# Optimization experiments

Measured on AMD Instinct MI355X. Metric: run time of the kernel, lower is better.

## Reference

```python
import jax, jax.numpy as jnp
import numpy as np

CI_SCALE = 1.0


def _rot_y(a):
    c, s = np.cos(a), np.sin(a)
    return np.array([[c, 0.0, s], [0.0, 1.0, 0.0], [-s, 0.0, c]], dtype=np.float32)


def setup_inputs() -> dict:
    key = jax.random.key(0)
    B, V, C, Hs, Ws = 1, 3, 32, 256, 256
    Ht, Wt, D = 128, 128, 48
    src_feat = jax.random.normal(key, (B, V, C, Hs, Ws), dtype=jnp.float32)
    # Realistic pinhole cameras so the plane-sweep warp lands in-frame.
    Ks = np.array([[200.0, 0.0, Ws / 2], [0.0, 200.0, Hs / 2], [0.0, 0.0, 1.0]], dtype=np.float32)
    Kt = np.array([[100.0, 0.0, Wt / 2], [0.0, 100.0, Ht / 2], [0.0, 0.0, 1.0]], dtype=np.float32)
    src_exts = np.zeros((B, V, 4, 4), dtype=np.float32)
    for i in range(V):
        R = _rot_y(0.1 * (i - (V - 1) / 2))
        src_exts[0, i, :3, :3] = R
        src_exts[0, i, :3, 3] = np.array([-0.3 * (i - (V - 1) / 2), 0.0, 0.0], dtype=np.float32)
        src_exts[0, i, 3, 3] = 1.0
    tar_exts = np.eye(4, dtype=np.float32)[None]
    return {
        "src_feat": src_feat,
        "src_exts": jnp.asarray(src_exts),
        "src_ints": jnp.asarray(np.broadcast_to(Ks, (B, V, 3, 3)).copy()),
        "tar_exts": jnp.asarray(tar_exts),
        "tar_ints": jnp.asarray(Kt[None].copy()),
        "near_far": jnp.broadcast_to(jnp.array([2.0, 6.0], dtype=jnp.float32).reshape(1, 2, 1, 1), (B, 2, Ht, Wt)),
        "num_depth": D,
    }


def _grid_sample_zeros(feat, grid):
    """Bilinear, padding_mode='zeros', align_corners=False.
    feat: (N,C,Hs,Ws); grid: (N,Hg,Wg,2) normalized -> (N,C,Hg,Wg)."""
    N, C, Hs, Ws = feat.shape
    gx = jnp.clip((grid[..., 0] + 1.0) * (Ws / 2) - 0.5, -1e6, 1e6)
    gy = jnp.clip((grid[..., 1] + 1.0) * (Hs / 2) - 0.5, -1e6, 1e6)
    x0f, y0f = jnp.floor(gx), jnp.floor(gy)
    wx, wy = gx - x0f, gy - y0f
    x0, y0 = x0f.astype(jnp.int32), y0f.astype(jnp.int32)
    x1, y1 = x0 + 1, y0 + 1
    b = jnp.arange(N)[:, None, None]

    def tap(yi, xi):
        valid = (xi >= 0) & (xi < Ws) & (yi >= 0) & (yi < Hs)
        v = feat[b, :, jnp.clip(yi, 0, Hs - 1), jnp.clip(xi, 0, Ws - 1)]  # (N,Hg,Wg,C)
        return v * valid[..., None]

    out = (tap(y0, x0) * ((1 - wy) * (1 - wx))[..., None]
           + tap(y0, x1) * ((1 - wy) * wx)[..., None]
           + tap(y1, x0) * (wy * (1 - wx))[..., None]
           + tap(y1, x1) * (wy * wx)[..., None])
    return jnp.transpose(out, (0, 3, 1, 2))


def _build_feature_volume(src_feat, src_exts, src_ints, tar_exts, tar_ints, depth_values):
    B, V, C, Hs, Ws = src_feat.shape
    D, Ht, Wt = depth_values.shape[1:]
    src_projs = src_ints @ src_exts[..., :3, :]                       # (B,V,3,4)
    tar34 = tar_ints @ tar_exts[:, :3, :]                             # (B,3,4)
    bottom = jnp.broadcast_to(jnp.array([0.0, 0.0, 0.0, 1.0], dtype=tar34.dtype).reshape(1, 1, 4), (B, 1, 4))
    tar_proj = jnp.concatenate([tar34, bottom], axis=1)               # (B,4,4)
    proj = (src_projs @ jnp.linalg.inv(tar_proj)[:, None]).reshape(B * V, 3, 4)
    xs = jnp.arange(Wt, dtype=src_feat.dtype) + 0.5
    ys = jnp.arange(Ht, dtype=src_feat.dtype) + 0.5
    gx, gy = jnp.meshgrid(xs, ys, indexing='xy')                      # (Ht,Wt)
    xyz = jnp.stack([gx, gy, jnp.ones_like(gx)], 0).reshape(3, Ht * Wt)
    dvals = jnp.broadcast_to(depth_values.reshape(B, 1, D, Ht * Wt), (B, V, D, Ht * Wt)).reshape(B * V, 1, D, Ht * Wt)
    p = proj[:, :, :3] @ xyz                                          # (BV,3,HW)
    p = p[:, :, None, :] * dvals + proj[:, :, 3:, None]               # (BV,3,D,HW)
    p = jnp.transpose(p, (0, 2, 3, 1))                                # (BV,D,HW,3)
    z = jnp.maximum(p[..., 2:3], 1e-6)
    g = p[..., :2] / z
    grid = jnp.stack([2 * g[..., 0] / Ws - 1, 2 * g[..., 1] / Hs - 1], -1)  # (BV,D,HW,2)
    warped = _grid_sample_zeros(src_feat.reshape(B * V, C, Hs, Ws), grid)   # (BV,C,D,HW)
    warped = warped.reshape(B, V, C, D, Ht, Wt)
    return jnp.var(warped, axis=1)                                    # (B,C,D,Ht,Wt), unbiased=False


def reference(src_feat, src_exts, src_ints, tar_exts, tar_ints, near_far, num_depth):
    B, _, Ht, Wt = near_far.shape
    t = jnp.linspace(0.0, 1.0, num_depth, dtype=near_far.dtype).reshape(1, num_depth, 1, 1)
    depth_values = near_far[:, :1] + (near_far[:, -1:] - near_far[:, :1]) * t   # (B,D,Ht,Wt)
    vol = _build_feature_volume(src_feat, src_exts, src_ints, tar_exts, tar_ints, depth_values)
    prob = jax.nn.softmax(-vol.mean(axis=1), axis=1)                  # (B,D,Ht,Wt)
    depth = jnp.sum(prob * depth_values, axis=1, keepdims=True)       # (B,1,Ht,Wt)
    var = jnp.sum(prob * jnp.square(depth_values - depth), axis=1, keepdims=True)
    half_ci = CI_SCALE * jnp.sqrt(jnp.maximum(var, 1e-12))
    ci = jnp.concatenate([jnp.maximum(depth - half_ci, depth_values[:, :1]),
                          jnp.minimum(depth + half_ci, depth_values[:, -1:])], axis=1)
    return depth, ci
```

## Files before the change

### kernel.cpp

```cpp
#include <hip/hip_runtime.h>
#include <math.h>

#define NV 3
#define NC 32
#define HS 256
#define WS 256
#define HT 128
#define WT 128
#define ND 48
#define NPIX (HT*WT)
#define HSP 259
#define WSP 259
#define ROW4 (WSP*8)
#define IMG4 (HSP*ROW4)
#define FEAT_T_ELEMS (NV*IMG4*4)
#define NB_INTERIOR (NV*HS)
#define NBORDER_PIX (3*(3*WSP + 3*HS))
#define NBORDER_F4  (NBORDER_PIX*8)
#define NB_BORDER   145

__device__ __forceinline__ float dpp_sum8(float x) {
    int v;
    v = __builtin_amdgcn_update_dpp(0, __float_as_int(x), 0xB1,  0xF, 0xF, true);
    x += __int_as_float(v);
    v = __builtin_amdgcn_update_dpp(0, __float_as_int(x), 0x4E,  0xF, 0xF, true);
    x += __int_as_float(v);
    v = __builtin_amdgcn_update_dpp(0, __float_as_int(x), 0x141, 0xF, 0xF, true);
    x += __int_as_float(v);
    return x;
}
__device__ __forceinline__ float dpp_max8(float x) {
    int v;
    v = __builtin_amdgcn_update_dpp(0, __float_as_int(x), 0xB1,  0xF, 0xF, true);
    x = fmaxf(x, __int_as_float(v));
    v = __builtin_amdgcn_update_dpp(0, __float_as_int(x), 0x4E,  0xF, 0xF, true);
    x = fmaxf(x, __int_as_float(v));
    v = __builtin_amdgcn_update_dpp(0, __float_as_int(x), 0x141, 0xF, 0xF, true);
    x = fmaxf(x, __int_as_float(v));
    return x;
}

__device__ __forceinline__ float4 f4mul(float4 a, float s) {
    return make_float4(a.x*s, a.y*s, a.z*s, a.w*s);
}
__device__ __forceinline__ float4 f4fma(float4 a, float s, float4 c) {
    return make_float4(fmaf(a.x,s,c.x), fmaf(a.y,s,c.y),
                       fmaf(a.z,s,c.z), fmaf(a.w,s,c.w));
}
__device__ __forceinline__ float4 f4fma2(float4 a, float4 c) {
    return make_float4(fmaf(a.x,a.x,c.x), fmaf(a.y,a.y,c.y),
                       fmaf(a.z,a.z,c.z), fmaf(a.w,a.w,c.w));
}
__device__ __forceinline__ float4 f4add(float4 a, float4 b) {
    return make_float4(a.x+b.x, a.y+b.y, a.z+b.z, a.w+b.w);
}

__global__ __launch_bounds__(256) void prep(
        const float* __restrict__ src, float* __restrict__ dstf,
        const float* __restrict__ src_exts,
        const float* __restrict__ src_ints,
        const float* __restrict__ tar_exts,
        const float* __restrict__ tar_ints,
        float* __restrict__ proj_out) {
    float4* dst = (float4*)dstf;
    int bid = blockIdx.x;
    if (bid < NB_INTERIOR) {
        int v  = bid >> 8;
        int y  = bid & 255;
        int q  = threadIdx.x & 7;
        int xg = threadIdx.x >> 3;
        const float* in = src + ((size_t)(v*NC + q*4))*HS*WS + (size_t)y*WS;
        float4* drow = dst + (size_t)(v*HSP + y+1)*ROW4 + 8 + q;
        #pragma unroll
        for (int half = 0; half < 2; half++) {
            int x0 = (xg + half*32)*4;
            float4 p0 = *(const float4*)(in + x0);
            float4 p1 = *(const float4*)(in + HS*WS   + x0);
            float4 p2 = *(const float4*)(in + 2*HS*WS + x0);
            float4 p3 = *(const float4*)(in + 3*HS*WS + x0);
            drow[(x0+0)*8] = make_float4(p0.x, p1.x, p2.x, p3.x);
            drow[(x0+1)*8] = make_float4(p0.y, p1.y, p2.y, p3.y);
            drow[(x0+2)*8] = make_float4(p0.z, p1.z, p2.z, p3.z);
            drow[(x0+3)*8] = make_float4(p0.w, p1.w, p2.w, p3.w);
        }
        return;
    }
    int t = (bid - NB_INTERIOR)*256 + threadIdx.x;
    if (t < NBORDER_F4) {
        int pixb = t >> 3, q = t & 7;
        int v = pixb / (NBORDER_PIX/3);
        int r = pixb - v*(NBORDER_PIX/3);
        int y, x;
        if (r < 3*WSP) {
            int band = r / WSP;
            y = (band == 0) ? 0 : (band == 1 ? 257 : 258);
            x = r - band*WSP;
        } else {
            int rr = r - 3*WSP;
            int band = rr >> 8;
            x = (band == 0) ? 0 : (band == 1 ? 257 : 258);
            y = 1 + (rr & 255);
        }
        dst[(v*HSP + y)*WSP*8 + x*8 + q] = make_float4(0.f,0.f,0.f,0.f);
    }
    if (bid == NB_INTERIOR && threadIdx.x == 0) {
        float Kt[9], Et[16];
        for (int i = 0; i < 9;  i++) Kt[i] = tar_ints[i];
        for (int i = 0; i < 16; i++) Et[i] = tar_exts[i];
        float T[12];
        for (int rI = 0; rI < 3; rI++)
            for (int col = 0; col < 4; col++) {
                float s = 0.f;
                for (int k = 0; k < 3; k++) s += Kt[rI*3+k] * Et[k*4+col];
                T[rI*4+col] = s;
            }
        float M[9]  = {T[0],T[1],T[2], T[4],T[5],T[6], T[8],T[9],T[10]};
        float tv[3] = {T[3],T[7],T[11]};
        float det = M[0]*(M[4]*M[8]-M[5]*M[7])
                  - M[1]*(M[3]*M[8]-M[5]*M[6])
                  + M[2]*(M[3]*M[7]-M[4]*M[6]);
        float id = 1.0f/det;
        float Mi[9];
        Mi[0] =  (M[4]*M[8]-M[5]*M[7])*id;
        Mi[1] = -(M[1]*M[8]-M[2]*M[7])*id;
        Mi[2] =  (M[1]*M[5]-M[2]*M[4])*id;
        Mi[3] = -(M[3]*M[8]-M[5]*M[6])*id;
        Mi[4] =  (M[0]*M[8]-M[2]*M[6])*id;
        Mi[5] = -(M[0]*M[5]-M[2]*M[3])*id;
        Mi[6] =  (M[3]*M[7]-M[4]*M[6])*id;
        Mi[7] = -(M[0]*M[7]-M[1]*M[6])*id;
        Mi[8] =  (M[0]*M[4]-M[1]*M[3])*id;
        float mt[3];
        for (int rI = 0; rI < 3; rI++)
            mt[rI] = -(Mi[rI*3+0]*tv[0] + Mi[rI*3+1]*tv[1] + Mi[rI*3+2]*tv[2]);
        float inv4[16] = {Mi[0],Mi[1],Mi[2],mt[0],
                          Mi[3],Mi[4],Mi[5],mt[1],
                          Mi[6],Mi[7],Mi[8],mt[2],
                          0.f,0.f,0.f,1.f};
        for (int v = 0; v < NV; v++) {
            const float* Ks = src_ints + v*9;
            const float* Ev = src_exts + v*16;
            float P34[12];
            for (int rI = 0; rI < 3; rI++)
                for (int col = 0; col < 4; col++) {
                    float s = 0.f;
                    for (int k = 0; k < 3; k++) s += Ks[rI*3+k] * Ev[k*4+col];
                    P34[rI*4+col] = s;
                }
            for (int rI = 0; rI < 3; rI++)
                for (int col = 0; col < 4; col++) {
                    float s = 0.f;
                    for (int k = 0; k < 4; k++) s += P34[rI*4+k] * inv4[k*4+col];
                    proj_out[v*12 + rI*4 + col] = s;
                }
        }
    }
}

__global__ __launch_bounds__(256, 6) void depth_main(
        const float4* __restrict__ featT,
        const float* __restrict__ proj,
        const float* __restrict__ near_far,
        float* __restrict__ out) {
    __shared__ float cl[8][56];

    const int tid  = threadIdx.x;
    const int w    = tid >> 6;
    const int lane = tid & 63;
    const int p    = lane >> 3;
    const int q    = lane & 7;

    const int lb  = ((blockIdx.x & 7) << 8) | (blockIdx.x >> 3);
    const int pix = lb*8 + p;
    const float cx = (pix & (WT-1)) + 0.5f;
    const float cy = (pix >> 7) + 0.5f;

    float rx[NV], ry[NV], rz[NV], tx[NV], ty[NV], tz[NV];
    #pragma unroll
    for (int v = 0; v < NV; v++) {
        const float* P = proj + v*12;
        rx[v] = P[0]*cx + P[1]*cy + P[2];  tx[v] = P[3];
        ry[v] = P[4]*cx + P[5]*cy + P[6];  ty[v] = P[7];
        rz[v] = P[8]*cx + P[9]*cy + P[10]; tz[v] = P[11];
    }

    const float nearv = near_far[pix];
    const float farv  = near_far[NPIX + pix];
    const float step  = (farv - nearv) * (1.0f/(ND-1));
    const float d0    = (float)(w*12);

    #pragma unroll 2
    for (int dd = 0; dd < 12; dd++) {
        const float dv = fmaf(step, d0 + (float)dd, nearv);
        float4 a4 = make_float4(0.f,0.f,0.f,0.f);
        float4 m4 = make_float4(0.f,0.f,0.f,0.f);
        #pragma unroll
        for (int v = 0; v < NV; v++) {
            float pxx = fmaf(rx[v], dv, tx[v]);
            float pyy = fmaf(ry[v], dv, ty[v]);
            float pzz = fmaf(rz[v], dv, tz[v]);
            float invz = __builtin_amdgcn_rcpf(fmaxf(pzz, 1e-6f));
            float sxp = fminf(fmaxf(fmaf(pxx, invz, 0.5f), 0.0f), 257.0f);
            float syp = fminf(fmaxf(fmaf(pyy, invz, 0.5f), 0.0f), 257.0f);
            float x0f = floorf(sxp), y0f = floorf(syp);
            float wx = sxp - x0f,   wy = syp - y0f;
            unsigned xi = (unsigned)(int)x0f;
            unsigned yi = (unsigned)(int)y0f;
            unsigned idx = (unsigned)(v*IMG4) + yi*ROW4 + xi*8u + (unsigned)q;
            float4 f00 = featT[idx];
            float4 f01 = featT[idx + 8];
            float4 f10 = featT[idx + ROW4];
            float4 f11 = featT[idx + ROW4 + 8];
            float w11 = wx*wy;
            float w10 = wy - w11;
            float w01 = wx - w11;
            float w00 = (1.0f - wx) - w10;
            float4 val = f4fma(f11, w11, f4fma(f10, w10,
                         f4fma(f01, w01, f4mul(f00, w00))));
            a4 = f4fma2(val, a4);
            m4 = f4add(m4, val);
        }
        float a  = (a4.x + a4.y) + (a4.z + a4.w);
        float m2 = (m4.x*m4.x + m4.y*m4.y) + (m4.z*m4.z + m4.w*m4.w);
        a  = dpp_sum8(a);
        m2 = dpp_sum8(m2);
        float cost = (a*(1.0f/3.0f) - m2*(1.0f/9.0f)) * (1.0f/32.0f);
        if (q == 0) cl[p][w*12 + dd] = cost;
    }

    __syncthreads();
    if (w != 0) return;

    float n[6], e[6];
    #pragma unroll
    for (int j = 0; j < 6; j++) n[j] = -cl[p][q + 8*j];
    float mx = n[0];
    #pragma unroll
    for (int j = 1; j < 6; j++) mx = fmaxf(mx, n[j]);
    mx = dpp_max8(mx);
    float s0 = 0.f, s1 = 0.f;
    #pragma unroll
    for (int j = 0; j < 6; j++) {
        float dvj = fmaf(step, (float)(q + 8*j), nearv);
        e[j] = __expf(n[j] - mx);
        s0 += e[j];
        s1 = fmaf(e[j], dvj, s1);
    }
    s0 = dpp_sum8(s0);
    s1 = dpp_sum8(s1);
    float depth = s1 / s0;
    float s2 = 0.f;
    #pragma unroll
    for (int j = 0; j < 6; j++) {
        float qd = fmaf(step, (float)(q + 8*j), nearv) - depth;
        s2 = fmaf(e[j]*qd, qd, s2);
    }
    s2 = dpp_sum8(s2);
    float var = s2 / s0;
    float hci = sqrtf(fmaxf(var, 1e-12f));
    if (q == 0) {
        out[pix]          = depth;
        out[NPIX + pix]   = fmaxf(depth - hci, nearv);
        out[2*NPIX + pix] = fminf(depth + hci, farv);
    }
}

extern "C" void kernel_launch(void* const* d_in, const int* in_sizes, int n_in,
                              void* d_out, int out_size, void* d_ws, size_t ws_size,
                              hipStream_t stream) {
    const float* src_feat = (const float*)d_in[0];
    const float* src_exts = (const float*)d_in[1];
    const float* src_ints = (const float*)d_in[2];
    const float* tar_exts = (const float*)d_in[3];
    const float* tar_ints = (const float*)d_in[4];
    const float* near_far = (const float*)d_in[5];
    float* out   = (float*)d_out;
    float* featT = (float*)d_ws;
    float* proj  = featT + FEAT_T_ELEMS;

    hipLaunchKernelGGL(prep, dim3(NB_INTERIOR + NB_BORDER), dim3(256), 0, stream,
                       src_feat, featT, src_exts, src_ints, tar_exts, tar_ints, proj);
    hipLaunchKernelGGL(depth_main, dim3(NPIX/8), dim3(256), 0, stream,
                       (const float4*)featT, proj, near_far, out);
}
```

Before: 120.1 us.

## Remap threads to 4 lanes per pixel with 8 channels each, 16 pixels per block

Each pixel is now served by 4 lanes that each handle 8 channels, read as two float4 halves, instead of 8 lanes with 4 channels each. Blocks grow to 512 threads covering 16 pixels, with 8 waves splitting the 48 depths six apiece. Per-view projection rows are recomputed inside the depth loop rather than kept in registers, and the softmax stage works on contiguous chunks of 12 depths per lane. This roughly halves the cross-lane reduction and index/weight work per channel and cuts register pressure. The cost is fewer distinct pixels' gathers in flight per wave and some repeated projection arithmetic.

```diff
diff --git a/kernel.cpp b/kernel.cpp
--- a/kernel.cpp
+++ b/kernel.cpp
@@ -19,23 +19,19 @@
 #define NBORDER_F4  (NBORDER_PIX*8)
 #define NB_BORDER   145
 
-__device__ __forceinline__ float dpp_sum8(float x) {
+__device__ __forceinline__ float dpp_sum4(float x) {
     int v;
-    v = __builtin_amdgcn_update_dpp(0, __float_as_int(x), 0xB1,  0xF, 0xF, true);
+    v = __builtin_amdgcn_update_dpp(0, __float_as_int(x), 0xB1, 0xF, 0xF, true);
     x += __int_as_float(v);
-    v = __builtin_amdgcn_update_dpp(0, __float_as_int(x), 0x4E,  0xF, 0xF, true);
-    x += __int_as_float(v);
-    v = __builtin_amdgcn_update_dpp(0, __float_as_int(x), 0x141, 0xF, 0xF, true);
+    v = __builtin_amdgcn_update_dpp(0, __float_as_int(x), 0x4E, 0xF, 0xF, true);
     x += __int_as_float(v);
     return x;
 }
-__device__ __forceinline__ float dpp_max8(float x) {
+__device__ __forceinline__ float dpp_max4(float x) {
     int v;
-    v = __builtin_amdgcn_update_dpp(0, __float_as_int(x), 0xB1,  0xF, 0xF, true);
+    v = __builtin_amdgcn_update_dpp(0, __float_as_int(x), 0xB1, 0xF, 0xF, true);
     x = fmaxf(x, __int_as_float(v));
-    v = __builtin_amdgcn_update_dpp(0, __float_as_int(x), 0x4E,  0xF, 0xF, true);
-    x = fmaxf(x, __int_as_float(v));
-    v = __builtin_amdgcn_update_dpp(0, __float_as_int(x), 0x141, 0xF, 0xF, true);
+    v = __builtin_amdgcn_update_dpp(0, __float_as_int(x), 0x4E, 0xF, 0xF, true);
     x = fmaxf(x, __int_as_float(v));
     return x;
 }
@@ -157,48 +153,43 @@
     }
 }
 
-__global__ __launch_bounds__(256, 6) void depth_main(
+__global__ __launch_bounds__(512, 8) void depth_main(
         const float4* __restrict__ featT,
         const float* __restrict__ proj,
         const float* __restrict__ near_far,
         float* __restrict__ out) {
-    __shared__ float cl[8][56];
+    __shared__ float cl[16][53];
 
     const int tid  = threadIdx.x;
     const int w    = tid >> 6;
     const int lane = tid & 63;
-    const int p    = lane >> 3;
-    const int q    = lane & 7;
-
-    const int lb  = ((blockIdx.x & 7) << 8) | (blockIdx.x >> 3);
-    const int pix = lb*8 + p;
+    const int p    = lane >> 2;
+    const int q    = lane & 3;
+
+    const int lb  = ((blockIdx.x & 7) << 7) | (blockIdx.x >> 3);
+    const int pix = lb*16 + p;
     const float cx = (pix & (WT-1)) + 0.5f;
     const float cy = (pix >> 7) + 0.5f;
-
-    float rx[NV], ry[NV], rz[NV], tx[NV], ty[NV], tz[NV];
-    #pragma unroll
-    for (int v = 0; v < NV; v++) {
-        const float* P = proj + v*12;
-        rx[v] = P[0]*cx + P[1]*cy + P[2];  tx[v] = P[3];
-        ry[v] = P[4]*cx + P[5]*cy + P[6];  ty[v] = P[7];
-        rz[v] = P[8]*cx + P[9]*cy + P[10]; tz[v] = P[11];
-    }
 
     const float nearv = near_far[pix];
     const float farv  = near_far[NPIX + pix];
     const float step  = (farv - nearv) * (1.0f/(ND-1));
-    const float d0    = (float)(w*12);
+    const float d0    = (float)(w*6);
 
     #pragma unroll 2
-    for (int dd = 0; dd < 12; dd++) {
+    for (int dd = 0; dd < 6; dd++) {
         const float dv = fmaf(step, d0 + (float)dd, nearv);
-        float4 a4 = make_float4(0.f,0.f,0.f,0.f);
-        float4 m4 = make_float4(0.f,0.f,0.f,0.f);
+        unsigned o0[NV], o1[NV];
+        float w00[NV], w01[NV], w10[NV], w11[NV];
         #pragma unroll
         for (int v = 0; v < NV; v++) {
-            float pxx = fmaf(rx[v], dv, tx[v]);
-            float pyy = fmaf(ry[v], dv, ty[v]);
-            float pzz = fmaf(rz[v], dv, tz[v]);
+            const float* P = proj + v*12;
+            float rxv = fmaf(P[0], cx, fmaf(P[1], cy, P[2]));
+            float ryv = fmaf(P[4], cx, fmaf(P[5], cy, P[6]));
+            float rzv = fmaf(P[8], cx, fmaf(P[9], cy, P[10]));
+            float pxx = fmaf(rxv, dv, P[3]);
+            float pyy = fmaf(ryv, dv, P[7]);
+            float pzz = fmaf(rzv, dv, P[11]);
             float invz = __builtin_amdgcn_rcpf(fmaxf(pzz, 1e-6f));
             float sxp = fminf(fmaxf(fmaf(pxx, invz, 0.5f), 0.0f), 257.0f);
             float syp = fminf(fmaxf(fmaf(pyy, invz, 0.5f), 0.0f), 257.0f);
@@ -207,55 +198,67 @@
             unsigned xi = (unsigned)(int)x0f;
             unsigned yi = (unsigned)(int)y0f;
             unsigned idx = (unsigned)(v*IMG4) + yi*ROW4 + xi*8u + (unsigned)q;
-            float4 f00 = featT[idx];
-            float4 f01 = featT[idx + 8];
-            float4 f10 = featT[idx + ROW4];
-            float4 f11 = featT[idx + ROW4 + 8];
-            float w11 = wx*wy;
-            float w10 = wy - w11;
-            float w01 = wx - w11;
-            float w00 = (1.0f - wx) - w10;
-            float4 val = f4fma(f11, w11, f4fma(f10, w10,
-                         f4fma(f01, w01, f4mul(f00, w00))));
-            a4 = f4fma2(val, a4);
-            m4 = f4add(m4, val);
-        }
-        float a  = (a4.x + a4.y) + (a4.z + a4.w);
-        float m2 = (m4.x*m4.x + m4.y*m4.y) + (m4.z*m4.z + m4.w*m4.w);
-        a  = dpp_sum8(a);
-        m2 = dpp_sum8(m2);
-        float cost = (a*(1.0f/3.0f) - m2*(1.0f/9.0f)) * (1.0f/32.0f);
-        if (q == 0) cl[p][w*12 + dd] = cost;
+            o0[v] = idx;
+            o1[v] = idx + ROW4;
+            float a11 = wx*wy;
+            w11[v] = a11;
+            w10[v] = wy - a11;
+            w01[v] = wx - a11;
+            w00[v] = (1.0f - wx) - (wy - a11);
+        }
+        float a_tot = 0.f, m2_tot = 0.f;
+        float4 a4 = make_float4(0.f,0.f,0.f,0.f);
+        #pragma unroll
+        for (int h = 0; h < 2; h++) {
+            float4 m4 = make_float4(0.f,0.f,0.f,0.f);
+            #pragma unroll
+            for (int v = 0; v < NV; v++) {
+                float4 f00 = featT[o0[v] + 4*h];
+                float4 f01 = featT[o0[v] + 4*h + 8];
+                float4 f10 = featT[o1[v] + 4*h];
+                float4 f11 = featT[o1[v] + 4*h + 8];
+                float4 val = f4fma(f11, w11[v], f4fma(f10, w10[v],
+                             f4fma(f01, w01[v], f4mul(f00, w00[v]))));
+                a4 = f4fma2(val, a4);
+                m4 = f4add(m4, val);
+            }
+            m2_tot += (m4.x*m4.x + m4.y*m4.y) + (m4.z*m4.z + m4.w*m4.w);
+        }
+        a_tot = (a4.x + a4.y) + (a4.z + a4.w);
+        a_tot  = dpp_sum4(a_tot);
+        m2_tot = dpp_sum4(m2_tot);
+        float cost = (a_tot*(1.0f/3.0f) - m2_tot*(1.0f/9.0f)) * (1.0f/32.0f);
+        if (q == 0) cl[p][w*6 + dd] = cost;
     }
 
     __syncthreads();
     if (w != 0) return;
 
-    float n[6], e[6];
-    #pragma unroll
-    for (int j = 0; j < 6; j++) n[j] = -cl[p][q + 8*j];
+    float n[12], e[12];
+    #pragma unroll
+    for (int j = 0; j < 12; j++) n[j] = -cl[p][q*12 + j];
     float mx = n[0];
     #pragma unroll
-    for (int j = 1; j < 6; j++) mx = fmaxf(mx, n[j]);
-    mx = dpp_max8(mx);
+    for (int j = 1; j < 12; j++) mx = fmaxf(mx, n[j]);
+    mx = dpp_max4(mx);
     float s0 = 0.f, s1 = 0.f;
     #pragma unroll
-    for (int j = 0; j < 6; j++) {
-        float dvj = fmaf(step, (float)(q + 8*j), nearv);
+    for (int j = 0; j < 12; j++) {
+        float dvj = fmaf(step, (float)(q*12 + j), nearv);
         e[j] = __expf(n[j] - mx);
         s0 += e[j];
         s1 = fmaf(e[j], dvj, s1);
     }
-    s0 = dpp_sum8(s0);
-    s1 = dpp_sum8(s1);
+    s0 = dpp_sum4(s0);
+    s1 = dpp_sum4(s1);
     float depth = s1 / s0;
     float s2 = 0.f;
     #pragma unroll
-    for (int j = 0; j < 6; j++) {
-        float qd = fmaf(step, (float)(q + 8*j), nearv) - depth;
+    for (int j = 0; j < 12; j++) {
+        float qd = fmaf(step, (float)(q*12 + j), nearv) - depth;
         s2 = fmaf(e[j]*qd, qd, s2);
     }
-    s2 = dpp_sum8(s2);
+    s2 = dpp_sum4(s2);
     float var = s2 / s0;
     float hci = sqrtf(fmaxf(var, 1e-12f));
     if (q == 0) {
@@ -280,6 +283,6 @@
 
     hipLaunchKernelGGL(prep, dim3(NB_INTERIOR + NB_BORDER), dim3(256), 0, stream,
                        src_feat, featT, src_exts, src_ints, tar_exts, tar_ints, proj);
-    hipLaunchKernelGGL(depth_main, dim3(NPIX/8), dim3(256), 0, stream,
+    hipLaunchKernelGGL(depth_main, dim3(NPIX/16), dim3(512), 0, stream,
                        (const float4*)featT, proj, near_far, out);
 }
```

After: 127.4 us. +6.1%, slower.

## Use 8 waves per block for depth sweep and split prep rows into halves

Applied to the files above, without the earlier changes.

The depth kernel now launches 512 threads (8 waves) per block. Each wave handles every 8th depth plane (6 planes) instead of a contiguous run of 12, so more depth work runs in parallel per pixel group. A __syncthreads now sits inside the depth loop, and the softmax reads a contiguous 6-entry slice per lane. The prep kernel uses twice as many blocks, each transposing half a row, for more memory-level parallelism. Risks are the extra per-iteration barrier, lower occupancy from the 512/4 launch bounds, and an LDS row padding of 49 that may cause bank conflicts.

```diff
diff --git a/kernel.cpp b/kernel.cpp
--- a/kernel.cpp
+++ b/kernel.cpp
@@ -14,7 +14,7 @@
 #define ROW4 (WSP*8)
 #define IMG4 (HSP*ROW4)
 #define FEAT_T_ELEMS (NV*IMG4*4)
-#define NB_INTERIOR (NV*HS)
+#define NB_INTERIOR (NV*HS*2)
 #define NBORDER_PIX (3*(3*WSP + 3*HS))
 #define NBORDER_F4  (NBORDER_PIX*8)
 #define NB_BORDER   145
@@ -65,24 +65,23 @@
     float4* dst = (float4*)dstf;
     int bid = blockIdx.x;
     if (bid < NB_INTERIOR) {
-        int v  = bid >> 8;
-        int y  = bid & 255;
-        int q  = threadIdx.x & 7;
-        int xg = threadIdx.x >> 3;
+        int v    = bid >> 9;
+        int rem  = bid & 511;
+        int y    = rem >> 1;
+        int half = rem & 1;
+        int q    = threadIdx.x & 7;
+        int xl   = threadIdx.x >> 3;
+        int x0   = half*128 + xl*4;
         const float* in = src + ((size_t)(v*NC + q*4))*HS*WS + (size_t)y*WS;
         float4* drow = dst + (size_t)(v*HSP + y+1)*ROW4 + 8 + q;
-        #pragma unroll
-        for (int half = 0; half < 2; half++) {
-            int x0 = (xg + half*32)*4;
-            float4 p0 = *(const float4*)(in + x0);
-            float4 p1 = *(const float4*)(in + HS*WS   + x0);
-            float4 p2 = *(const float4*)(in + 2*HS*WS + x0);
-            float4 p3 = *(const float4*)(in + 3*HS*WS + x0);
-            drow[(x0+0)*8] = make_float4(p0.x, p1.x, p2.x, p3.x);
-            drow[(x0+1)*8] = make_float4(p0.y, p1.y, p2.y, p3.y);
-            drow[(x0+2)*8] = make_float4(p0.z, p1.z, p2.z, p3.z);
-            drow[(x0+3)*8] = make_float4(p0.w, p1.w, p2.w, p3.w);
-        }
+        float4 p0 = *(const float4*)(in + x0);
+        float4 p1 = *(const float4*)(in + HS*WS   + x0);
+        float4 p2 = *(const float4*)(in + 2*HS*WS + x0);
+        float4 p3 = *(const float4*)(in + 3*HS*WS + x0);
+        drow[(x0+0)*8] = make_float4(p0.x, p1.x, p2.x, p3.x);
+        drow[(x0+1)*8] = make_float4(p0.y, p1.y, p2.y, p3.y);
+        drow[(x0+2)*8] = make_float4(p0.z, p1.z, p2.z, p3.z);
+        drow[(x0+3)*8] = make_float4(p0.w, p1.w, p2.w, p3.w);
         return;
     }
     int t = (bid - NB_INTERIOR)*256 + threadIdx.x;
@@ -157,12 +156,12 @@
     }
 }
 
-__global__ __launch_bounds__(256, 6) void depth_main(
+__global__ __launch_bounds__(512, 4) void depth_main(
         const float4* __restrict__ featT,
         const float* __restrict__ proj,
         const float* __restrict__ near_far,
         float* __restrict__ out) {
-    __shared__ float cl[8][56];
+    __shared__ float cl[8][49];
 
     const int tid  = threadIdx.x;
     const int w    = tid >> 6;
@@ -179,19 +178,18 @@
     #pragma unroll
     for (int v = 0; v < NV; v++) {
         const float* P = proj + v*12;
-        rx[v] = P[0]*cx + P[1]*cy + P[2];  tx[v] = P[3];
-        ry[v] = P[4]*cx + P[5]*cy + P[6];  ty[v] = P[7];
-        rz[v] = P[8]*cx + P[9]*cy + P[10]; tz[v] = P[11];
+        rx[v] = fmaf(P[0], cx, fmaf(P[1], cy, P[2]));  tx[v] = P[3];
+        ry[v] = fmaf(P[4], cx, fmaf(P[5], cy, P[6]));  ty[v] = P[7];
+        rz[v] = fmaf(P[8], cx, fmaf(P[9], cy, P[10])); tz[v] = P[11];
     }
 
     const float nearv = near_far[pix];
     const float farv  = near_far[NPIX + pix];
     const float step  = (farv - nearv) * (1.0f/(ND-1));
-    const float d0    = (float)(w*12);
-
-    #pragma unroll 2
-    for (int dd = 0; dd < 12; dd++) {
-        const float dv = fmaf(step, d0 + (float)dd, nearv);
+
+    for (int dd = 0; dd < 6; dd++) {
+        const int   d  = dd*8 + w;
+        const float dv = fmaf(step, (float)d, nearv);
         float4 a4 = make_float4(0.f,0.f,0.f,0.f);
         float4 m4 = make_float4(0.f,0.f,0.f,0.f);
         #pragma unroll
@@ -225,15 +223,15 @@
         a  = dpp_sum8(a);
         m2 = dpp_sum8(m2);
         float cost = (a*(1.0f/3.0f) - m2*(1.0f/9.0f)) * (1.0f/32.0f);
-        if (q == 0) cl[p][w*12 + dd] = cost;
-    }
-
-    __syncthreads();
+        if (q == 0) cl[p][d] = cost;
+        __syncthreads();
+    }
+
     if (w != 0) return;
 
     float n[6], e[6];
     #pragma unroll
-    for (int j = 0; j < 6; j++) n[j] = -cl[p][q + 8*j];
+    for (int j = 0; j < 6; j++) n[j] = -cl[p][q*6 + j];
     float mx = n[0];
     #pragma unroll
     for (int j = 1; j < 6; j++) mx = fmaxf(mx, n[j]);
@@ -241,7 +239,7 @@
     float s0 = 0.f, s1 = 0.f;
     #pragma unroll
     for (int j = 0; j < 6; j++) {
-        float dvj = fmaf(step, (float)(q + 8*j), nearv);
+        float dvj = fmaf(step, (float)(q*6 + j), nearv);
         e[j] = __expf(n[j] - mx);
         s0 += e[j];
         s1 = fmaf(e[j], dvj, s1);
@@ -252,7 +250,7 @@
     float s2 = 0.f;
     #pragma unroll
     for (int j = 0; j < 6; j++) {
-        float qd = fmaf(step, (float)(q + 8*j), nearv) - depth;
+        float qd = fmaf(step, (float)(q*6 + j), nearv) - depth;
         s2 = fmaf(e[j]*qd, qd, s2);
     }
     s2 = dpp_sum8(s2);
@@ -280,6 +278,6 @@
 
     hipLaunchKernelGGL(prep, dim3(NB_INTERIOR + NB_BORDER), dim3(256), 0, stream,
                        src_feat, featT, src_exts, src_ints, tar_exts, tar_ints, proj);
-    hipLaunchKernelGGL(depth_main, dim3(NPIX/8), dim3(256), 0, stream,
+    hipLaunchKernelGGL(depth_main, dim3(NPIX/8), dim3(512), 0, stream,
                        (const float4*)featT, proj, near_far, out);
 }
```

Result: no change. 121.6 us (+1.3%).
